# Kernel optimization log

Measured on AMD Instinct MI355X. Metric: run time of the kernel, lower is better.

## Reference

```python
import jax, jax.numpy as jnp
import numpy as np
import math

HIDDEN = 1024
HEADS = 16
HEAD = HIDDEN // HEADS  # 64
SCALE_BASE = 512.0


def _gammas(heads):
    # 1 - exp(linspace(log(1/32), log(1/512), heads))
    return 1.0 - jnp.exp(jnp.linspace(math.log(1.0 / 32.0), math.log(1.0 / 512.0), heads))


def _xpos(x, downscale):
    # x: [B, H, S, d]  (same head_size d for every head -> shared tables)
    S, d = x.shape[2], x.shape[3]
    half = d // 2
    base_scale = (jnp.arange(0, d, 2, dtype=jnp.float32) + 0.4 * d) / (1.4 * d)  # [half]
    pos = jnp.arange(S, dtype=jnp.float32)
    scale = base_scale[None, :] ** (pos / SCALE_BASE)[:, None]  # [S, half]
    if downscale:
        scale = 1.0 / scale
    inv_freq = 1.0 / (10000.0 ** (jnp.arange(half, dtype=jnp.float32) / half))
    sinusoid = pos[:, None] * inv_freq[None, :]  # [S, half]
    # duplicate-interleave (each column repeated twice)
    sin = jnp.repeat(jnp.sin(sinusoid) * scale, 2, axis=-1)  # [S, d]
    cos = jnp.repeat(jnp.cos(sinusoid) * scale, 2, axis=-1)  # [S, d]
    x1 = x[..., ::2]
    x2 = x[..., 1::2]
    rot = jnp.stack([-x2, x1], axis=-1).reshape(x.shape)  # rotate_every_two
    return x * cos + rot * sin


def _decay_mask(S, gammas):
    # D[h, n, m] = gamma_h^(n-m) for n >= m else 0
    n = jnp.arange(S)[:, None]
    m = jnp.arange(S)[None, :]
    diff = (n - m).astype(jnp.float32)
    mask = (n >= m)
    pw = jnp.maximum(diff, 0.0)[None, :, :]  # avoid overflow on negative diffs
    return jnp.where(mask[None, :, :], gammas[:, None, None] ** pw, 0.0)  # [H, S, S]


def retention_forward(Q, K, V):
    B, S, _ = Q.shape
    # split heads: [B, S, HIDDEN] -> [B, H, S, HEAD]
    def split(x, hd):
        return x.reshape(B, S, HEADS, hd).transpose(0, 2, 1, 3)
    q = _xpos(split(Q, HEAD), downscale=False)
    k = _xpos(split(K, HEAD), downscale=True)
    v = split(V, HEAD)
    D = _decay_mask(S, _gammas(HEADS).astype(Q.dtype))  # [H, S, S]
    scores = jnp.einsum('bhsd,bhtd->bhst', q, k) * D[None]
    out = jnp.einsum('bhst,bhtd->bhsd', scores, v)
    return out.transpose(0, 2, 1, 3).reshape(B, S, HEADS * HEAD)


def setup_inputs() -> dict:
    key = jax.random.key(0)
    kq, kk, kv = jax.random.split(key, 3)
    B, S = 2, 2048
    return {
        'Q': jax.random.normal(kq, (B, S, HIDDEN), dtype=jnp.float32),
        'K': jax.random.normal(kk, (B, S, HIDDEN), dtype=jnp.float32),
        'V': jax.random.normal(kv, (B, S, HIDDEN), dtype=jnp.float32),
    }


def reference(Q, K, V):
    return retention_forward(Q, K, V)
```

## Files before the change

### kernel.cpp

```cpp
#include <hip/hip_runtime.h>
#include <hip/hip_bf16.h>
#include <math.h>

#define B_  2
#define S_  2048
#define H_  16
#define D_  64
#define SST 40

typedef __attribute__((ext_vector_type(8))) short bf16x8_t;
typedef __attribute__((ext_vector_type(4))) float f32x4_t;

__device__ __forceinline__ unsigned short f2bf(float f) {
    __hip_bfloat16 h = __float2bfloat16(f);
    return __builtin_bit_cast(unsigned short, h);
}

__device__ __forceinline__ void async16(const unsigned short* g, unsigned short* l) {
    __builtin_amdgcn_global_load_lds(
        (const __attribute__((address_space(1))) unsigned int*)g,
        (__attribute__((address_space(3))) unsigned int*)l, 16, 0, 0);
}

#define WAITV2 asm volatile("s_waitcnt vmcnt(2)" ::: "memory")
#define WAITV0 asm volatile("s_waitcnt vmcnt(0)" ::: "memory")
#define BAR    asm volatile("s_barrier" ::: "memory")

__global__ __launch_bounds__(256) void prep_kernel(const float* __restrict__ Q,
                                                   const float* __restrict__ K,
                                                   const float* __restrict__ V,
                                                   unsigned short* __restrict__ qb,
                                                   unsigned short* __restrict__ kb,
                                                   unsigned short* __restrict__ vt) {
    __shared__ float  tile[64 * 65];
    __shared__ float4 rotq[4 * 32];
    __shared__ float  gl[4 * 16 * 2];
    int t   = threadIdx.x;
    int bid = blockIdx.x;

    if (t < 128) {
        int sl = t >> 5, i = t & 31;
        int s  = (bid * 4 + sl) & 2047;
        float pos = (float)s;
        float bsc  = (2.0f * (float)i + 25.6f) / 89.6f;
        float xsc  = exp2f(log2f(bsc) * pos * (1.0f / 512.0f));
        float invf = exp2f(-(float)i * (13.287712379549449f / 32.0f));
        float ang  = pos * invf;
        float kq = rintf(ang * 0.15915494309189535f);
        float rr = fmaf(kq, -6.2831853071795865f, ang);
        float sn = sinf(rr), cs = cosf(rr);
        float rxs = 1.0f / xsc;
        rotq[sl * 32 + i] = make_float4(cs * xsc, sn * xsc, cs * rxs, sn * rxs);
    } else {
        int u  = t - 128;
        int sl = u >> 5, hh = (u >> 1) & 15, pm = u & 1;
        int s  = (bid * 4 + sl) & 2047;
        float lnv = -3.4657359027997265f + (float)hh * (-0.18483924814931874f);
        float l2g = log2f(1.0f - expf(lnv));
        gl[(sl * 16 + hh) * 2 + pm] = exp2f((pm ? -(float)s : (float)s) * l2g);
    }
    __syncthreads();

    {
        int hh = t >> 4, i8 = t & 15;
#pragma unroll
        for (int j = 0; j < 4; ++j) {
            int r = bid * 4 + j;
            float4 r0 = rotq[j * 32 + 2 * i8];
            float4 r1 = rotq[j * 32 + 2 * i8 + 1];
            float gx = gl[(j * 16 + hh) * 2 + 0];
            float gy = gl[(j * 16 + hh) * 2 + 1];

            long idx = (long)r * 1024 + t * 4;
            float4 xq = *(const float4*)(Q + idx);
            float4 xk = *(const float4*)(K + idx);

            float cq0 = r0.x * gx, sq0 = r0.y * gx;
            float ck0 = r0.z * gy, sk0 = r0.w * gy;
            float cq1 = r1.x * gx, sq1 = r1.y * gx;
            float ck1 = r1.z * gy, sk1 = r1.w * gy;

            float q0 = xq.x * cq0 - xq.y * sq0, q1 = xq.y * cq0 + xq.x * sq0;
            float q2 = xq.z * cq1 - xq.w * sq1, q3 = xq.w * cq1 + xq.z * sq1;
            float k0 = xk.x * ck0 - xk.y * sk0, k1 = xk.y * ck0 + xk.x * sk0;
            float k2 = xk.z * ck1 - xk.w * sk1, k3 = xk.w * ck1 + xk.z * sk1;

            *(uint2*)(qb + idx) = make_uint2((unsigned)f2bf(q0) | ((unsigned)f2bf(q1) << 16),
                                             (unsigned)f2bf(q2) | ((unsigned)f2bf(q3) << 16));
            *(uint2*)(kb + idx) = make_uint2((unsigned)f2bf(k0) | ((unsigned)f2bf(k1) << 16),
                                             (unsigned)f2bf(k2) | ((unsigned)f2bf(k3) << 16));
        }
    }
    __syncthreads();

    {
        int bh = bid & 31;
        int b = bh >> 4, hh = bh & 15;
        int s0 = (bid >> 5) * 64;

#pragma unroll
        for (int it = 0; it < 4; ++it) {
            int f  = it * 256 + t;
            int sl = f >> 4;
            int d4 = f & 15;
            float4 v = *(const float4*)(V + ((long)(b * S_ + s0 + sl)) * 1024 + hh * 64 + d4 * 4);
            tile[sl * 65 + d4 * 4 + 0] = v.x;
            tile[sl * 65 + d4 * 4 + 1] = v.y;
            tile[sl * 65 + d4 * 4 + 2] = v.z;
            tile[sl * 65 + d4 * 4 + 3] = v.w;
        }
        __syncthreads();
        int d = t >> 2, c = t & 3;
        unsigned int pk[8];
#pragma unroll
        for (int jj = 0; jj < 8; ++jj) {
            float f0 = tile[(c * 16 + 2 * jj + 0) * 65 + d];
            float f1 = tile[(c * 16 + 2 * jj + 1) * 65 + d];
            pk[jj] = (unsigned int)f2bf(f0) | ((unsigned int)f2bf(f1) << 16);
        }
        unsigned short* outp = vt + ((long)(bh * 64 + d)) * S_ + s0 + c * 16;
        ((uint4*)outp)[0] = make_uint4(pk[0], pk[1], pk[2], pk[3]);
        ((uint4*)outp)[1] = make_uint4(pk[4], pk[5], pk[6], pk[7]);
    }
}

__global__ __launch_bounds__(512, 4) void retention_kernel(const unsigned short* __restrict__ qb,
                                                           const unsigned short* __restrict__ kb,
                                                           const unsigned short* __restrict__ vt,
                                                           float* __restrict__ out) {
    __shared__ __align__(16) unsigned short KV[16384];
    __shared__ __align__(16) unsigned short Ss[8][32 * SST];
    unsigned short* K0 = KV;
    unsigned short* V0 = KV + 4096;
    unsigned short* K1 = KV + 8192;
    unsigned short* V1 = KV + 12288;

    int t = threadIdx.x;
    int w = t >> 6, lane = t & 63, quad = lane >> 4, l16 = lane & 15;
    int qw = w & 3;
    int p  = w >> 2;

    int i   = blockIdx.x;
    int bb0 = i & 1;
    int h4  = (i >> 1) & 15;
    int c3  = (i >> 5) & 7;
    int b8  = (i >> 8) & 1;
    int par = bb0 ^ b8;
    int g   = par ? (15 - h4) : h4;
    int bh  = c3 | (b8 << 3) | (bb0 << 4);
    int b = bh >> 4, hh = bh & 15;

    int q0w  = g * 128 + qw * 32;
    int dkt  = 2 * g + (qw >> 1);
    int odd  = qw & 1;
    int kvend = 2 * g + 2;

    const unsigned short* qB = qb + ((long)(b * S_ + q0w)) * 1024 + hh * 64;
    const unsigned short* kB = kb + ((long)(b * S_)) * 1024 + hh * 64;
    const unsigned short* vB = vt + (long)bh * 64 * S_;

    bf16x8_t aQ[2][2];
#pragma unroll
    for (int m = 0; m < 2; ++m)
#pragma unroll
        for (int kk = 0; kk < 2; ++kk)
            aQ[m][kk] = *(const bf16x8_t*)(qB + (long)(m * 16 + l16) * 1024 + kk * 32 + quad * 8);

    f32x4_t acc[2][4];
#pragma unroll
    for (int m = 0; m < 2; ++m)
#pragma unroll
        for (int nd = 0; nd < 4; ++nd) acc[m][nd] = (f32x4_t){0.f, 0.f, 0.f, 0.f};

    auto stage = [&](unsigned short* Kd, unsigned short* Vd, int kt) {
        const unsigned short* kSrc = kB + (long)kt * 64 * 1024;
        const unsigned short* vSrc = vB + kt * 64;
        int row = w * 8 + (lane >> 3);
        int c   = (lane & 7) ^ (row & 7);
        async16(kSrc + (long)row * 1024 + c * 8, Kd + w * 512);
        async16(vSrc + (long)row * S_ + c * 8, Vd + w * 512);
    };

    auto computeHalf = [&](const unsigned short* Kt, const unsigned short* Vt, bool diag) {
        f32x4_t sc[2][2];
#pragma unroll
        for (int m = 0; m < 2; ++m)
#pragma unroll
            for (int ntl = 0; ntl < 2; ++ntl) sc[m][ntl] = (f32x4_t){0.f, 0.f, 0.f, 0.f};

#pragma unroll
        for (int kk = 0; kk < 2; ++kk)
#pragma unroll
            for (int ntl = 0; ntl < 2; ++ntl) {
                int krow = p * 32 + ntl * 16 + l16;
                bf16x8_t bk = *(const bf16x8_t*)&Kt[krow * 64 +
                                                   (((kk * 4 + quad) ^ (krow & 7)) * 8)];
                sc[0][ntl] = __builtin_amdgcn_mfma_f32_16x16x32_bf16(aQ[0][kk], bk, sc[0][ntl], 0, 0, 0);
                sc[1][ntl] = __builtin_amdgcn_mfma_f32_16x16x32_bf16(aQ[1][kk], bk, sc[1][ntl], 0, 0, 0);
            }

        unsigned short* ssw = Ss[w];
        if (!diag) {
#pragma unroll
            for (int m = 0; m < 2; ++m)
#pragma unroll
                for (int ntl = 0; ntl < 2; ++ntl)
#pragma unroll
                    for (int r = 0; r < 4; ++r)
                        ssw[(m * 16 + quad * 4 + r) * SST + ntl * 16 + l16] = f2bf(sc[m][ntl][r]);
        } else {
#pragma unroll
            for (int m = 0; m < 2; ++m)
#pragma unroll
                for (int ntl = 0; ntl < 2; ++ntl) {
                    int dlt = (m - ntl) * 16;
#pragma unroll
                    for (int r = 0; r < 4; ++r) {
                        int rr = quad * 4 + r;
                        float v = ((rr + dlt) >= l16) ? sc[m][ntl][r] : 0.0f;
                        ssw[(m * 16 + rr) * SST + ntl * 16 + l16] = f2bf(v);
                    }
                }
        }

        bf16x8_t aS0 = *(const bf16x8_t*)&ssw[(0 * 16 + l16) * SST + quad * 8];
        bf16x8_t aS1 = *(const bf16x8_t*)&ssw[(1 * 16 + l16) * SST + quad * 8];
#pragma unroll
        for (int nd = 0; nd < 4; ++nd) {
            int vrow = nd * 16 + l16;
            bf16x8_t bv = *(const bf16x8_t*)&Vt[vrow * 64 +
                                               (((p * 4 + quad) ^ (vrow & 7)) * 8)];
            acc[0][nd] = __builtin_amdgcn_mfma_f32_16x16x32_bf16(aS0, bv, acc[0][nd], 0, 0, 0);
            acc[1][nd] = __builtin_amdgcn_mfma_f32_16x16x32_bf16(aS1, bv, acc[1][nd], 0, 0, 0);
        }
    };

    stage(K0, V0, 0);
    for (int kt = 0; kt < kvend; kt += 2) {
        stage(K1, V1, kt + 1);
        WAITV2;
        BAR;
        if (kt < dkt || (kt == dkt && p <= odd)) computeHalf(K0, V0, kt == dkt && p == odd);
        BAR;

        if (kt + 2 < kvend) { stage(K0, V0, kt + 2); WAITV2; }
        else                { WAITV0; }
        BAR;
        if (kt + 1 < dkt || (kt + 1 == dkt && p <= odd))
            computeHalf(K1, V1, kt + 1 == dkt && p == odd);
        BAR;
    }

    float* red = (float*)KV;
    if (p == 1) {
#pragma unroll
        for (int m = 0; m < 2; ++m)
#pragma unroll
            for (int nd = 0; nd < 4; ++nd)
#pragma unroll
                for (int r = 0; r < 4; ++r)
                    red[qw * 2048 + (m * 16 + quad * 4 + r) * 64 + nd * 16 + l16] = acc[m][nd][r];
    }
    BAR;
    if (p == 0) {
#pragma unroll
        for (int m = 0; m < 2; ++m)
#pragma unroll
            for (int nd = 0; nd < 4; ++nd)
#pragma unroll
                for (int r = 0; r < 4; ++r) {
                    int row = q0w + m * 16 + quad * 4 + r;
                    float v = acc[m][nd][r] +
                              red[qw * 2048 + (m * 16 + quad * 4 + r) * 64 + nd * 16 + l16];
                    out[((long)(b * S_ + row)) * 1024 + hh * 64 + nd * 16 + l16] = v;
                }
    }
}

extern "C" void kernel_launch(void* const* d_in, const int* in_sizes, int n_in,
                              void* d_out, int out_size, void* d_ws, size_t ws_size,
                              hipStream_t stream) {
    const float* Q = (const float*)d_in[0];
    const float* K = (const float*)d_in[1];
    const float* V = (const float*)d_in[2];
    float* out = (float*)d_out;

    const size_t perBuf = (size_t)B_ * H_ * S_ * D_;
    unsigned short* qb = (unsigned short*)d_ws;
    unsigned short* kb = qb + perBuf;
    unsigned short* vt = kb + perBuf;

    hipLaunchKernelGGL(prep_kernel, dim3(1024), dim3(256), 0, stream, Q, K, V, qb, kb, vt);
    hipLaunchKernelGGL(retention_kernel, dim3(512), dim3(512), 0, stream, qb, kb, vt, out);
}
```

Measured before the change: 125.4 us.

## Replace quadratic retention with chunked linear-state recurrence across four kernels

```diff
diff --git a/kernel.cpp b/kernel.cpp
--- a/kernel.cpp
+++ b/kernel.cpp
@@ -6,7 +6,6 @@
 #define S_  2048
 #define H_  16
 #define D_  64
-#define SST 40
 
 typedef __attribute__((ext_vector_type(8))) short bf16x8_t;
 typedef __attribute__((ext_vector_type(4))) float f32x4_t;
@@ -15,24 +14,15 @@
     __hip_bfloat16 h = __float2bfloat16(f);
     return __builtin_bit_cast(unsigned short, h);
 }
-
-__device__ __forceinline__ void async16(const unsigned short* g, unsigned short* l) {
-    __builtin_amdgcn_global_load_lds(
-        (const __attribute__((address_space(1))) unsigned int*)g,
-        (__attribute__((address_space(3))) unsigned int*)l, 16, 0, 0);
-}
-
-#define WAITV2 asm volatile("s_waitcnt vmcnt(2)" ::: "memory")
-#define WAITV0 asm volatile("s_waitcnt vmcnt(0)" ::: "memory")
-#define BAR    asm volatile("s_barrier" ::: "memory")
-
-__global__ __launch_bounds__(256) void prep_kernel(const float* __restrict__ Q,
-                                                   const float* __restrict__ K,
-                                                   const float* __restrict__ V,
-                                                   unsigned short* __restrict__ qb,
-                                                   unsigned short* __restrict__ kb,
-                                                   unsigned short* __restrict__ vt) {
-    __shared__ float  tile[64 * 65];
+__device__ __forceinline__ float bf2f(unsigned short u) {
+    unsigned int x = ((unsigned int)u) << 16;
+    return __builtin_bit_cast(float, x);
+}
+
+__global__ __launch_bounds__(256) void prep1_kernel(const float* __restrict__ Q,
+                                                    const float* __restrict__ K,
+                                                    unsigned short* __restrict__ qb,
+                                                    unsigned short* __restrict__ kb) {
     __shared__ float4 rotq[4 * 32];
     __shared__ float  gl[4 * 16 * 2];
     int t   = threadIdx.x;
@@ -61,220 +51,205 @@
     }
     __syncthreads();
 
-    {
-        int hh = t >> 4, i8 = t & 15;
-#pragma unroll
-        for (int j = 0; j < 4; ++j) {
-            int r = bid * 4 + j;
-            float4 r0 = rotq[j * 32 + 2 * i8];
-            float4 r1 = rotq[j * 32 + 2 * i8 + 1];
-            float gx = gl[(j * 16 + hh) * 2 + 0];
-            float gy = gl[(j * 16 + hh) * 2 + 1];
-
-            long idx = (long)r * 1024 + t * 4;
-            float4 xq = *(const float4*)(Q + idx);
-            float4 xk = *(const float4*)(K + idx);
-
-            float cq0 = r0.x * gx, sq0 = r0.y * gx;
-            float ck0 = r0.z * gy, sk0 = r0.w * gy;
-            float cq1 = r1.x * gx, sq1 = r1.y * gx;
-            float ck1 = r1.z * gy, sk1 = r1.w * gy;
-
-            float q0 = xq.x * cq0 - xq.y * sq0, q1 = xq.y * cq0 + xq.x * sq0;
-            float q2 = xq.z * cq1 - xq.w * sq1, q3 = xq.w * cq1 + xq.z * sq1;
-            float k0 = xk.x * ck0 - xk.y * sk0, k1 = xk.y * ck0 + xk.x * sk0;
-            float k2 = xk.z * ck1 - xk.w * sk1, k3 = xk.w * ck1 + xk.z * sk1;
-
-            *(uint2*)(qb + idx) = make_uint2((unsigned)f2bf(q0) | ((unsigned)f2bf(q1) << 16),
-                                             (unsigned)f2bf(q2) | ((unsigned)f2bf(q3) << 16));
-            *(uint2*)(kb + idx) = make_uint2((unsigned)f2bf(k0) | ((unsigned)f2bf(k1) << 16),
-                                             (unsigned)f2bf(k2) | ((unsigned)f2bf(k3) << 16));
-        }
+    int hh = t >> 4, i8 = t & 15;
+#pragma unroll
+    for (int j = 0; j < 4; ++j) {
+        int r = bid * 4 + j;
+        float4 r0 = rotq[j * 32 + 2 * i8];
+        float4 r1 = rotq[j * 32 + 2 * i8 + 1];
+        float gx = gl[(j * 16 + hh) * 2 + 0];
+        float gy = gl[(j * 16 + hh) * 2 + 1];
+
+        long idx = (long)r * 1024 + t * 4;
+        float4 xq = *(const float4*)(Q + idx);
+        float4 xk = *(const float4*)(K + idx);
+
+        float cq0 = r0.x * gx, sq0 = r0.y * gx;
+        float ck0 = r0.z * gy, sk0 = r0.w * gy;
+        float cq1 = r1.x * gx, sq1 = r1.y * gx;
+        float ck1 = r1.z * gy, sk1 = r1.w * gy;
+
+        float q0 = xq.x * cq0 - xq.y * sq0, q1 = xq.y * cq0 + xq.x * sq0;
+        float q2 = xq.z * cq1 - xq.w * sq1, q3 = xq.w * cq1 + xq.z * sq1;
+        float k0 = xk.x * ck0 - xk.y * sk0, k1 = xk.y * ck0 + xk.x * sk0;
+        float k2 = xk.z * ck1 - xk.w * sk1, k3 = xk.w * ck1 + xk.z * sk1;
+
+        *(uint2*)(qb + idx) = make_uint2((unsigned)f2bf(q0) | ((unsigned)f2bf(q1) << 16),
+                                         (unsigned)f2bf(q2) | ((unsigned)f2bf(q3) << 16));
+        *(uint2*)(kb + idx) = make_uint2((unsigned)f2bf(k0) | ((unsigned)f2bf(k1) << 16),
+                                         (unsigned)f2bf(k2) | ((unsigned)f2bf(k3) << 16));
+    }
+}
+
+__global__ __launch_bounds__(256) void prep2_kernel(const float* __restrict__ V,
+                                                    const unsigned short* __restrict__ kb,
+                                                    unsigned short* __restrict__ vt,
+                                                    unsigned short* __restrict__ kt) {
+    __shared__ float tile[64 * 65];
+    int t   = threadIdx.x;
+    int bid = blockIdx.x;
+    bool isK = bid >= 1024;
+    int vb = isK ? bid - 1024 : bid;
+    int bh = vb & 31;
+    int b = bh >> 4, hh = bh & 15;
+    int s0 = (vb >> 5) * 64;
+
+#pragma unroll
+    for (int it = 0; it < 4; ++it) {
+        int f  = it * 256 + t;
+        int sl = f >> 4;
+        int d4 = f & 15;
+        long a = ((long)(b * S_ + s0 + sl)) * 1024 + hh * 64 + d4 * 4;
+        float f0, f1, f2, f3;
+        if (!isK) {
+            float4 v = *(const float4*)(V + a);
+            f0 = v.x; f1 = v.y; f2 = v.z; f3 = v.w;
+        } else {
+            uint2 u = *(const uint2*)(kb + a);
+            f0 = bf2f((unsigned short)(u.x & 0xffff));
+            f1 = bf2f((unsigned short)(u.x >> 16));
+            f2 = bf2f((unsigned short)(u.y & 0xffff));
+            f3 = bf2f((unsigned short)(u.y >> 16));
+        }
+        tile[sl * 65 + d4 * 4 + 0] = f0;
+        tile[sl * 65 + d4 * 4 + 1] = f1;
+        tile[sl * 65 + d4 * 4 + 2] = f2;
+        tile[sl * 65 + d4 * 4 + 3] = f3;
     }
     __syncthreads();
-
-    {
-        int bh = bid & 31;
-        int b = bh >> 4, hh = bh & 15;
-        int s0 = (bid >> 5) * 64;
-
-#pragma unroll
-        for (int it = 0; it < 4; ++it) {
-            int f  = it * 256 + t;
-            int sl = f >> 4;
-            int d4 = f & 15;
-            float4 v = *(const float4*)(V + ((long)(b * S_ + s0 + sl)) * 1024 + hh * 64 + d4 * 4);
-            tile[sl * 65 + d4 * 4 + 0] = v.x;
-            tile[sl * 65 + d4 * 4 + 1] = v.y;
-            tile[sl * 65 + d4 * 4 + 2] = v.z;
-            tile[sl * 65 + d4 * 4 + 3] = v.w;
-        }
-        __syncthreads();
-        int d = t >> 2, c = t & 3;
-        unsigned int pk[8];
-#pragma unroll
-        for (int jj = 0; jj < 8; ++jj) {
-            float f0 = tile[(c * 16 + 2 * jj + 0) * 65 + d];
-            float f1 = tile[(c * 16 + 2 * jj + 1) * 65 + d];
-            pk[jj] = (unsigned int)f2bf(f0) | ((unsigned int)f2bf(f1) << 16);
-        }
-        unsigned short* outp = vt + ((long)(bh * 64 + d)) * S_ + s0 + c * 16;
-        ((uint4*)outp)[0] = make_uint4(pk[0], pk[1], pk[2], pk[3]);
-        ((uint4*)outp)[1] = make_uint4(pk[4], pk[5], pk[6], pk[7]);
-    }
-}
-
-__global__ __launch_bounds__(512, 4) void retention_kernel(const unsigned short* __restrict__ qb,
-                                                           const unsigned short* __restrict__ kb,
-                                                           const unsigned short* __restrict__ vt,
-                                                           float* __restrict__ out) {
-    __shared__ __align__(16) unsigned short KV[16384];
-    __shared__ __align__(16) unsigned short Ss[8][32 * SST];
-    unsigned short* K0 = KV;
-    unsigned short* V0 = KV + 4096;
-    unsigned short* K1 = KV + 8192;
-    unsigned short* V1 = KV + 12288;
-
+    int d = t >> 2, c = t & 3;
+    unsigned int pk[8];
+#pragma unroll
+    for (int jj = 0; jj < 8; ++jj) {
+        float f0 = tile[(c * 16 + 2 * jj + 0) * 65 + d];
+        float f1 = tile[(c * 16 + 2 * jj + 1) * 65 + d];
+        pk[jj] = (unsigned int)f2bf(f0) | ((unsigned int)f2bf(f1) << 16);
+    }
+    unsigned short* outp = (isK ? kt : vt) + ((long)(bh * 64 + d)) * S_ + s0 + c * 16;
+    ((uint4*)outp)[0] = make_uint4(pk[0], pk[1], pk[2], pk[3]);
+    ((uint4*)outp)[1] = make_uint4(pk[4], pk[5], pk[6], pk[7]);
+}
+
+__global__ __launch_bounds__(256) void state_kernel(const unsigned short* __restrict__ kt,
+                                                    const unsigned short* __restrict__ vt,
+                                                    unsigned short* __restrict__ Sg) {
     int t = threadIdx.x;
     int w = t >> 6, lane = t & 63, quad = lane >> 4, l16 = lane & 15;
-    int qw = w & 3;
-    int p  = w >> 2;
-
-    int i   = blockIdx.x;
-    int bb0 = i & 1;
-    int h4  = (i >> 1) & 15;
-    int c3  = (i >> 5) & 7;
-    int b8  = (i >> 8) & 1;
-    int par = bb0 ^ b8;
-    int g   = par ? (15 - h4) : h4;
-    int bh  = c3 | (b8 << 3) | (bb0 << 4);
+    int bh = blockIdx.x;
+    const unsigned short* ktB = kt + (long)bh * 64 * S_;
+    const unsigned short* vtB = vt + (long)bh * 64 * S_;
+
+    f32x4_t accS[4];
+#pragma unroll
+    for (int dkt = 0; dkt < 4; ++dkt) accS[dkt] = (f32x4_t){0.f, 0.f, 0.f, 0.f};
+
+    for (int j = 0; j < 32; ++j) {
+        if (j > 0) {
+            unsigned short* Sp = Sg + ((long)(bh * 32 + j)) * 4096;
+#pragma unroll
+            for (int dkt = 0; dkt < 4; ++dkt)
+#pragma unroll
+                for (int r = 0; r < 4; ++r)
+                    Sp[(w * 16 + quad * 4 + r) * 64 + dkt * 16 + l16] = f2bf(accS[dkt][r]);
+        }
+        bf16x8_t aV[2], bK[4][2];
+#pragma unroll
+        for (int sst = 0; sst < 2; ++sst)
+            aV[sst] = *(const bf16x8_t*)(vtB + (long)(w * 16 + l16) * S_ + j * 64 + sst * 32 + quad * 8);
+#pragma unroll
+        for (int dkt = 0; dkt < 4; ++dkt)
+#pragma unroll
+            for (int sst = 0; sst < 2; ++sst)
+                bK[dkt][sst] = *(const bf16x8_t*)(ktB + (long)(dkt * 16 + l16) * S_ + j * 64 + sst * 32 + quad * 8);
+#pragma unroll
+        for (int dkt = 0; dkt < 4; ++dkt)
+#pragma unroll
+            for (int sst = 0; sst < 2; ++sst)
+                accS[dkt] = __builtin_amdgcn_mfma_f32_16x16x32_bf16(aV[sst], bK[dkt][sst], accS[dkt], 0, 0, 0);
+    }
+}
+
+__global__ __launch_bounds__(256) void outc_kernel(const unsigned short* __restrict__ qb,
+                                                   const unsigned short* __restrict__ kb,
+                                                   const unsigned short* __restrict__ vt,
+                                                   const unsigned short* __restrict__ Sg,
+                                                   float* __restrict__ out) {
+    __shared__ __align__(16) unsigned short strip[4][16 * 72];
+    int t = threadIdx.x;
+    int w = t >> 6, lane = t & 63, quad = lane >> 4, l16 = lane & 15;
+    int idx = blockIdx.x;
+    int bh  = idx & 31;
+    int tch = idx >> 5;
     int b = bh >> 4, hh = bh & 15;
 
-    int q0w  = g * 128 + qw * 32;
-    int dkt  = 2 * g + (qw >> 1);
-    int odd  = qw & 1;
-    int kvend = 2 * g + 2;
-
-    const unsigned short* qB = qb + ((long)(b * S_ + q0w)) * 1024 + hh * 64;
-    const unsigned short* kB = kb + ((long)(b * S_)) * 1024 + hh * 64;
-    const unsigned short* vB = vt + (long)bh * 64 * S_;
-
-    bf16x8_t aQ[2][2];
-#pragma unroll
-    for (int m = 0; m < 2; ++m)
-#pragma unroll
-        for (int kk = 0; kk < 2; ++kk)
-            aQ[m][kk] = *(const bf16x8_t*)(qB + (long)(m * 16 + l16) * 1024 + kk * 32 + quad * 8);
-
-    f32x4_t acc[2][4];
-#pragma unroll
-    for (int m = 0; m < 2; ++m)
-#pragma unroll
-        for (int nd = 0; nd < 4; ++nd) acc[m][nd] = (f32x4_t){0.f, 0.f, 0.f, 0.f};
-
-    auto stage = [&](unsigned short* Kd, unsigned short* Vd, int kt) {
-        const unsigned short* kSrc = kB + (long)kt * 64 * 1024;
-        const unsigned short* vSrc = vB + kt * 64;
-        int row = w * 8 + (lane >> 3);
-        int c   = (lane & 7) ^ (row & 7);
-        async16(kSrc + (long)row * 1024 + c * 8, Kd + w * 512);
-        async16(vSrc + (long)row * S_ + c * 8, Vd + w * 512);
-    };
-
-    auto computeHalf = [&](const unsigned short* Kt, const unsigned short* Vt, bool diag) {
-        f32x4_t sc[2][2];
-#pragma unroll
-        for (int m = 0; m < 2; ++m)
-#pragma unroll
-            for (int ntl = 0; ntl < 2; ++ntl) sc[m][ntl] = (f32x4_t){0.f, 0.f, 0.f, 0.f};
-
-#pragma unroll
-        for (int kk = 0; kk < 2; ++kk)
-#pragma unroll
-            for (int ntl = 0; ntl < 2; ++ntl) {
-                int krow = p * 32 + ntl * 16 + l16;
-                bf16x8_t bk = *(const bf16x8_t*)&Kt[krow * 64 +
-                                                   (((kk * 4 + quad) ^ (krow & 7)) * 8)];
-                sc[0][ntl] = __builtin_amdgcn_mfma_f32_16x16x32_bf16(aQ[0][kk], bk, sc[0][ntl], 0, 0, 0);
-                sc[1][ntl] = __builtin_amdgcn_mfma_f32_16x16x32_bf16(aQ[1][kk], bk, sc[1][ntl], 0, 0, 0);
+    const unsigned short* qB = qb + ((long)(b * S_ + tch * 64)) * 1024 + hh * 64;
+    const unsigned short* kB = kb + ((long)(b * S_ + tch * 64)) * 1024 + hh * 64;
+    const unsigned short* vB = vt + (long)bh * 64 * S_ + tch * 64;
+    const unsigned short* SB = Sg + ((long)(bh * 32 + tch)) * 4096;
+
+    bf16x8_t aQ[2];
+#pragma unroll
+    for (int kk = 0; kk < 2; ++kk)
+        aQ[kk] = *(const bf16x8_t*)(qB + (long)(w * 16 + l16) * 1024 + kk * 32 + quad * 8);
+
+    f32x4_t accO[4];
+#pragma unroll
+    for (int dvt = 0; dvt < 4; ++dvt) accO[dvt] = (f32x4_t){0.f, 0.f, 0.f, 0.f};
+
+    if (tch > 0) {
+#pragma unroll
+        for (int dvt = 0; dvt < 4; ++dvt)
+#pragma unroll
+            for (int kk = 0; kk < 2; ++kk) {
+                bf16x8_t bS = *(const bf16x8_t*)(SB + (dvt * 16 + l16) * 64 + kk * 32 + quad * 8);
+                accO[dvt] = __builtin_amdgcn_mfma_f32_16x16x32_bf16(aQ[kk], bS, accO[dvt], 0, 0, 0);
             }
-
-        unsigned short* ssw = Ss[w];
-        if (!diag) {
-#pragma unroll
-            for (int m = 0; m < 2; ++m)
-#pragma unroll
-                for (int ntl = 0; ntl < 2; ++ntl)
-#pragma unroll
-                    for (int r = 0; r < 4; ++r)
-                        ssw[(m * 16 + quad * 4 + r) * SST + ntl * 16 + l16] = f2bf(sc[m][ntl][r]);
-        } else {
-#pragma unroll
-            for (int m = 0; m < 2; ++m)
-#pragma unroll
-                for (int ntl = 0; ntl < 2; ++ntl) {
-                    int dlt = (m - ntl) * 16;
-#pragma unroll
-                    for (int r = 0; r < 4; ++r) {
-                        int rr = quad * 4 + r;
-                        float v = ((rr + dlt) >= l16) ? sc[m][ntl][r] : 0.0f;
-                        ssw[(m * 16 + rr) * SST + ntl * 16 + l16] = f2bf(v);
-                    }
-                }
-        }
-
-        bf16x8_t aS0 = *(const bf16x8_t*)&ssw[(0 * 16 + l16) * SST + quad * 8];
-        bf16x8_t aS1 = *(const bf16x8_t*)&ssw[(1 * 16 + l16) * SST + quad * 8];
-#pragma unroll
-        for (int nd = 0; nd < 4; ++nd) {
-            int vrow = nd * 16 + l16;
-            bf16x8_t bv = *(const bf16x8_t*)&Vt[vrow * 64 +
-                                               (((p * 4 + quad) ^ (vrow & 7)) * 8)];
-            acc[0][nd] = __builtin_amdgcn_mfma_f32_16x16x32_bf16(aS0, bv, acc[0][nd], 0, 0, 0);
-            acc[1][nd] = __builtin_amdgcn_mfma_f32_16x16x32_bf16(aS1, bv, acc[1][nd], 0, 0, 0);
-        }
-    };
-
-    stage(K0, V0, 0);
-    for (int kt = 0; kt < kvend; kt += 2) {
-        stage(K1, V1, kt + 1);
-        WAITV2;
-        BAR;
-        if (kt < dkt || (kt == dkt && p <= odd)) computeHalf(K0, V0, kt == dkt && p == odd);
-        BAR;
-
-        if (kt + 2 < kvend) { stage(K0, V0, kt + 2); WAITV2; }
-        else                { WAITV0; }
-        BAR;
-        if (kt + 1 < dkt || (kt + 1 == dkt && p <= odd))
-            computeHalf(K1, V1, kt + 1 == dkt && p == odd);
-        BAR;
-    }
-
-    float* red = (float*)KV;
-    if (p == 1) {
-#pragma unroll
-        for (int m = 0; m < 2; ++m)
-#pragma unroll
-            for (int nd = 0; nd < 4; ++nd)
-#pragma unroll
-                for (int r = 0; r < 4; ++r)
-                    red[qw * 2048 + (m * 16 + quad * 4 + r) * 64 + nd * 16 + l16] = acc[m][nd][r];
-    }
-    BAR;
-    if (p == 0) {
-#pragma unroll
-        for (int m = 0; m < 2; ++m)
-#pragma unroll
-            for (int nd = 0; nd < 4; ++nd)
-#pragma unroll
-                for (int r = 0; r < 4; ++r) {
-                    int row = q0w + m * 16 + quad * 4 + r;
-                    float v = acc[m][nd][r] +
-                              red[qw * 2048 + (m * 16 + quad * 4 + r) * 64 + nd * 16 + l16];
-                    out[((long)(b * S_ + row)) * 1024 + hh * 64 + nd * 16 + l16] = v;
-                }
-    }
+    }
+
+    unsigned short* sw = strip[w];
+    for (int st = w + 1; st < 4; ++st)
+        *(uint2*)&sw[l16 * 72 + st * 16 + quad * 4] = make_uint2(0u, 0u);
+
+    for (int st = 0; st <= w; ++st) {
+        f32x4_t pp = (f32x4_t){0.f, 0.f, 0.f, 0.f};
+#pragma unroll
+        for (int kk = 0; kk < 2; ++kk) {
+            bf16x8_t aK = *(const bf16x8_t*)(kB + (long)(st * 16 + l16) * 1024 + kk * 32 + quad * 8);
+            pp = __builtin_amdgcn_mfma_f32_16x16x32_bf16(aK, aQ[kk], pp, 0, 0, 0);
+        }
+        if (st == w) {
+#pragma unroll
+            for (int r = 0; r < 4; ++r)
+                if (quad * 4 + r > l16) pp[r] = 0.0f;
+        }
+        uint2 pk2;
+        pk2.x = (unsigned)f2bf(pp[0]) | ((unsigned)f2bf(pp[1]) << 16);
+        pk2.y = (unsigned)f2bf(pp[2]) | ((unsigned)f2bf(pp[3]) << 16);
+        *(uint2*)&sw[l16 * 72 + st * 16 + quad * 4] = pk2;
+    }
+
+    bf16x8_t aP0 = *(const bf16x8_t*)&sw[l16 * 72 + 0 * 32 + quad * 8];
+#pragma unroll
+    for (int dvt = 0; dvt < 4; ++dvt) {
+        bf16x8_t bV0 = *(const bf16x8_t*)(vB + (long)(dvt * 16 + l16) * S_ + 0 * 32 + quad * 8);
+        accO[dvt] = __builtin_amdgcn_mfma_f32_16x16x32_bf16(aP0, bV0, accO[dvt], 0, 0, 0);
+    }
+    if (w >= 2) {
+        bf16x8_t aP1 = *(const bf16x8_t*)&sw[l16 * 72 + 1 * 32 + quad * 8];
+#pragma unroll
+        for (int dvt = 0; dvt < 4; ++dvt) {
+            bf16x8_t bV1 = *(const bf16x8_t*)(vB + (long)(dvt * 16 + l16) * S_ + 1 * 32 + quad * 8);
+            accO[dvt] = __builtin_amdgcn_mfma_f32_16x16x32_bf16(aP1, bV1, accO[dvt], 0, 0, 0);
+        }
+    }
+
+#pragma unroll
+    for (int dvt = 0; dvt < 4; ++dvt)
+#pragma unroll
+        for (int r = 0; r < 4; ++r) {
+            int row = tch * 64 + w * 16 + quad * 4 + r;
+            out[((long)(b * S_ + row)) * 1024 + hh * 64 + dvt * 16 + l16] = accO[dvt][r];
+        }
 }
 
 extern "C" void kernel_launch(void* const* d_in, const int* in_sizes, int n_in,
@@ -289,7 +264,11 @@
     unsigned short* qb = (unsigned short*)d_ws;
     unsigned short* kb = qb + perBuf;
     unsigned short* vt = kb + perBuf;
-
-    hipLaunchKernelGGL(prep_kernel, dim3(1024), dim3(256), 0, stream, Q, K, V, qb, kb, vt);
-    hipLaunchKernelGGL(retention_kernel, dim3(512), dim3(512), 0, stream, qb, kb, vt, out);
-}
+    unsigned short* kt = vt + perBuf;
+    unsigned short* Sg = kt + perBuf;
+
+    hipLaunchKernelGGL(prep1_kernel, dim3(1024), dim3(256), 0, stream, Q, K, qb, kb);
+    hipLaunchKernelGGL(prep2_kernel, dim3(2048), dim3(256), 0, stream, V, kb, vt, kt);
+    hipLaunchKernelGGL(state_kernel, dim3(32),   dim3(256), 0, stream, kt, vt, Sg);
+    hipLaunchKernelGGL(outc_kernel,  dim3(1024), dim3(256), 0, stream, qb, kb, vt, Sg, out);
+}
```

After: 157.5 us. +25.6%, slower.
